# Kernel optimization log

Hardware: AMD Instinct MI355X
Metric: run time of the kernel (lower is better)

The kernel has to match this reference:

```python
import jax, jax.numpy as jnp
import numpy as np

NHEAD, HEAD_DIM = 10, 10
TEMPERATURE = 1.0
INV_SQRT_HD = np.float32(1.0 / np.sqrt(HEAD_DIM))


def setup_inputs() -> dict:
    key = jax.random.key(0)
    ks = jax.random.split(key, 6)
    B, nhid, L = 4, 128, 1024
    D = NHEAD * HEAD_DIM  # 100
    x = jax.random.normal(ks[0], (B, nhid, L, 1), dtype=jnp.float32)
    edge_matrix = jax.random.randint(ks[1], (B, L, L), 0, 2, dtype=jnp.int32)
    wq_w = jax.random.normal(ks[2], (D, nhid), dtype=jnp.float32) * 0.05
    wq_b = jnp.zeros((D,), jnp.float32)
    wedge_w = jax.random.normal(ks[3], (2 * HEAD_DIM,), dtype=jnp.float32) * 0.1
    wedge_b = jnp.zeros((1,), jnp.float32)
    wo_w = jax.random.normal(ks[4], (nhid, D), dtype=jnp.float32) * 0.05
    wo_b = jnp.zeros((nhid,), jnp.float32)
    return dict(x=x, edge_matrix=edge_matrix, wq_w=wq_w, wq_b=wq_b,
                wedge_w=wedge_w, wedge_b=wedge_b, wo_w=wo_w, wo_b=wo_b)


def reference(x, edge_matrix, wq_w, wq_b, wedge_w, wedge_b, wo_w, wo_b):
    B, nhid, L, _ = x.shape
    # WQ: 1x1 conv == per-position linear over channels
    q = jnp.einsum('bhl,ch->bcl', x[..., 0], wq_w) + wq_b[None, :, None]  # (B, nhead*hd, L)
    # source overwrites k and v with q (WK/WV dead code): k == v == q
    k = q.reshape(B, NHEAD, HEAD_DIM, L).transpose(0, 1, 3, 2)  # (B, nhead, L, hd)
    # WEDGE(Linear(2*hd,1)) over concat[k_i, k_j] == w1.k_i + w2.k_j + b (exact same math,
    # avoids materializing the O(L^2 * 2*hd) a_input tensor)
    s_i = jnp.einsum('bnld,d->bnl', k, wedge_w[:HEAD_DIM])
    s_j = jnp.einsum('bnld,d->bnl', k, wedge_w[HEAD_DIM:])
    alpha = (s_i[:, :, :, None] + s_j[:, :, None, :] + wedge_b[0]) * INV_SQRT_HD  # (B,nhead,L,L)
    alpha = jnp.where(edge_matrix[:, None, :, :] == 0, jnp.float32(-1e15), alpha)
    alpha = jax.nn.softmax(alpha, axis=-1) / TEMPERATURE  # dropout: identity at eval
    att = jnp.einsum('bnij,bnjd->bnid', alpha, k)  # v == k; (B, nhead, L, hd)
    # faithful to torch: raw row-major view(B, -1, L, 1) that scrambles (head,pos) ordering
    att = att.reshape(B, NHEAD * HEAD_DIM, L, 1)
    ret = jnp.einsum('bcl,oc->bol', att[..., 0], wo_w) + wo_b[None, :, None]
    ret = ret[..., None]  # (B, nhid, L, 1)
    return ret, alpha.reshape(B * NHEAD, L, L)
```

## Files before the change

### kernel.cpp

```cpp
#include <hip/hip_runtime.h>

#define BB   4
#define NHID 128
#define LL   1024
#define NH   10
#define HD   10
#define DD   100
#define SCALE 0.31622776601683794f

typedef float vfloat4 __attribute__((ext_vector_type(4)));

__global__ __launch_bounds__(256) void k_qproj(
    const float* __restrict__ x, const float* __restrict__ wq_w,
    const float* __restrict__ wq_b, float* __restrict__ kbuf) {
  const int l  = blockIdx.x * 256 + threadIdx.x;
  const int c0 = blockIdx.y * 2;
  const int b  = blockIdx.z;
  float acc0 = wq_b[c0], acc1 = wq_b[c0 + 1];
  const float* xb = x + (size_t)b * NHID * LL + l;
  const float* w0 = wq_w + (size_t)c0 * NHID;
  const float* w1 = w0 + NHID;
  #pragma unroll 8
  for (int h = 0; h < NHID; ++h) {
    float xv = xb[(size_t)h * LL];
    acc0 += w0[h] * xv;
    acc1 += w1[h] * xv;
  }
  {
    int c = c0, n = c / HD, d = c % HD;
    kbuf[(((size_t)(b * NH + n)) * LL + l) * HD + d] = acc0;
  }
  {
    int c = c0 + 1, n = c / HD, d = c % HD;
    kbuf[(((size_t)(b * NH + n)) * LL + l) * HD + d] = acc1;
  }
}

__global__ __launch_bounds__(256) void k_edgeproj(
    const float* __restrict__ kbuf, const float* __restrict__ we_w,
    float* __restrict__ esj) {
  const int idx = blockIdx.x * 256 + threadIdx.x;
  const float* kr = kbuf + (size_t)idx * HD;
  float s2 = 0.f;
  #pragma unroll
  for (int d = 0; d < HD; ++d) s2 += kr[d] * we_w[HD + d];
  esj[idx] = __expf(s2 * SCALE);
}

__global__ __launch_bounds__(256) void k_attn(
    const float* __restrict__ kbuf, const float* __restrict__ esj,
    const int* __restrict__ edge,
    float* __restrict__ alpha_out, float* __restrict__ att) {
  const int t    = threadIdx.x;
  const int lane = t & 63;
  const int wid  = t >> 6;
  const int blk  = blockIdx.x;
  const int rt   = blk & 63;
  const int bn   = blk >> 6;
  const int b    = bn / NH;
  const int i0   = rt * 16 + wid * 4;

  __shared__ float ks[LL * HD];
  {
    const float4* src = (const float4*)(kbuf + (size_t)bn * (LL * HD));
    float4* dst = (float4*)ks;
    for (int idx = t; idx < (LL * HD) / 4; idx += 256) dst[idx] = src[idx];
  }
  float  esv[16];
  float4 esv4[4];
  {
    const float* sp = esj + (size_t)bn * LL;
    #pragma unroll
    for (int m = 0; m < 16; ++m) esv[m] = sp[m * 64 + lane];
    const float4* sp4 = (const float4*)sp;
    #pragma unroll
    for (int m = 0; m < 4; ++m) esv4[m] = sp4[m * 64 + lane];
  }
  __syncthreads();

  const int* ebase = edge + (size_t)b * LL * LL;

  float part[4][HD];
  float denom[4];
  #pragma unroll
  for (int r = 0; r < 4; ++r) {
    denom[r] = 0.f;
    #pragma unroll
    for (int d = 0; d < HD; ++d) part[r][d] = 0.f;
  }
  #pragma unroll
  for (int m = 0; m < 16; ++m) {
    const float* kr = ks + (m * 64 + lane) * HD;
    float2 kv0 = *(const float2*)(kr + 0);
    float2 kv1 = *(const float2*)(kr + 2);
    float2 kv2 = *(const float2*)(kr + 4);
    float2 kv3 = *(const float2*)(kr + 6);
    float2 kv4 = *(const float2*)(kr + 8);
    const float es = esv[m];
    #pragma unroll
    for (int r = 0; r < 4; ++r) {
      int e = ebase[(size_t)(i0 + r) * LL + m * 64 + lane];
      float au = e ? es : 0.f;
      denom[r] += au;
      part[r][0] += au * kv0.x; part[r][1] += au * kv0.y;
      part[r][2] += au * kv1.x; part[r][3] += au * kv1.y;
      part[r][4] += au * kv2.x; part[r][5] += au * kv2.y;
      part[r][6] += au * kv3.x; part[r][7] += au * kv3.y;
      part[r][8] += au * kv4.x; part[r][9] += au * kv4.y;
    }
  }
  float inv[4];
  #pragma unroll
  for (int r = 0; r < 4; ++r) {
    float s = denom[r];
    #pragma unroll
    for (int sft = 32; sft >= 1; sft >>= 1) s += __shfl_xor(s, sft, 64);
    inv[r] = __builtin_amdgcn_rcpf(s);
  }

  float* ap = alpha_out + ((size_t)bn * LL + i0) * LL;
  #pragma unroll
  for (int m = 0; m < 4; ++m) {
    #pragma unroll
    for (int r = 0; r < 4; ++r) {
      int4 e = ((const int4*)(ebase + (size_t)(i0 + r) * LL))[m * 64 + lane];
      vfloat4 a;
      a.x = e.x ? esv4[m].x * inv[r] : 0.f;
      a.y = e.y ? esv4[m].y * inv[r] : 0.f;
      a.z = e.z ? esv4[m].z * inv[r] : 0.f;
      a.w = e.w ? esv4[m].w * inv[r] : 0.f;
      vfloat4* dst = (vfloat4*)(ap + (size_t)r * LL) + m * 64 + lane;
      __builtin_nontemporal_store(a, dst);
    }
  }

  const bool b5 = (lane & 32) != 0;
  const bool b4 = (lane & 16) != 0;
  const bool b3 = (lane & 8) != 0;
  const bool b2 = (lane & 4) != 0;
  #pragma unroll
  for (int r = 0; r < 4; ++r) {
    float pv[16];
    #pragma unroll
    for (int d = 0; d < HD; ++d) pv[d] = part[r][d];
    #pragma unroll
    for (int d = HD; d < 16; ++d) pv[d] = 0.f;
    #pragma unroll
    for (int i = 0; i < 8; ++i) {
      float snd = b5 ? pv[i] : pv[i + 8];
      float kp  = b5 ? pv[i + 8] : pv[i];
      pv[i] = kp + __shfl_xor(snd, 32, 64);
    }
    #pragma unroll
    for (int i = 0; i < 4; ++i) {
      float snd = b4 ? pv[i] : pv[i + 4];
      float kp  = b4 ? pv[i + 4] : pv[i];
      pv[i] = kp + __shfl_xor(snd, 16, 64);
    }
    #pragma unroll
    for (int i = 0; i < 2; ++i) {
      float snd = b3 ? pv[i] : pv[i + 2];
      float kp  = b3 ? pv[i + 2] : pv[i];
      pv[i] = kp + __shfl_xor(snd, 8, 64);
    }
    {
      float snd = b2 ? pv[0] : pv[1];
      float kp  = b2 ? pv[1] : pv[0];
      pv[0] = kp + __shfl_xor(snd, 4, 64);
    }
    pv[0] += __shfl_xor(pv[0], 2, 64);
    pv[0] += __shfl_xor(pv[0], 1, 64);
    float g = __shfl(pv[0], lane * 4, 64);
    if (lane < HD)
      att[((size_t)bn * LL + (i0 + r)) * HD + lane] = g * inv[r];
  }
}

__global__ __launch_bounds__(256) void k_out(
    const float* __restrict__ att, const float* __restrict__ wo_w,
    const float* __restrict__ wo_b, float* __restrict__ ret) {
  const int l  = blockIdx.x * 256 + threadIdx.x;
  const int o0 = blockIdx.y * 4;
  const int b  = blockIdx.z;
  const float* ab = att + (size_t)b * (DD * LL);
  float acc[4];
  #pragma unroll
  for (int oo = 0; oo < 4; ++oo) acc[oo] = wo_b[o0 + oo];
  for (int c = 0; c < DD; ++c) {
    float a = ab[(size_t)c * LL + l];
    #pragma unroll
    for (int oo = 0; oo < 4; ++oo) acc[oo] += wo_w[(size_t)(o0 + oo) * DD + c] * a;
  }
  #pragma unroll
  for (int oo = 0; oo < 4; ++oo)
    ret[((size_t)b * NHID + o0 + oo) * LL + l] = acc[oo];
}

extern "C" void kernel_launch(void* const* d_in, const int* in_sizes, int n_in,
                              void* d_out, int out_size, void* d_ws, size_t ws_size,
                              hipStream_t stream) {
  (void)in_sizes; (void)n_in; (void)out_size; (void)ws_size;
  const float* x    = (const float*)d_in[0];
  const int*   edge = (const int*)d_in[1];
  const float* wq_w = (const float*)d_in[2];
  const float* wq_b = (const float*)d_in[3];
  const float* we_w = (const float*)d_in[4];
  const float* wo_w = (const float*)d_in[6];
  const float* wo_b = (const float*)d_in[7];

  float* out       = (float*)d_out;
  float* ret_out   = out;
  float* alpha_out = out + (size_t)BB * NHID * LL;

  float* ws   = (float*)d_ws;
  float* kbuf = ws;
  float* esj  = kbuf + (size_t)BB * NH * LL * HD;
  float* att  = esj + (size_t)BB * NH * LL;

  dim3 g1(LL / 256, DD / 2, BB);
  k_qproj<<<g1, 256, 0, stream>>>(x, wq_w, wq_b, kbuf);

  k_edgeproj<<<(BB * NH * LL) / 256, 256, 0, stream>>>(kbuf, we_w, esj);

  k_attn<<<BB * NH * (LL / 16), 256, 0, stream>>>(kbuf, esj, edge, alpha_out, att);

  dim3 g3(LL / 256, NHID / 4, BB);
  k_out<<<g3, 256, 0, stream>>>(att, wo_w, wo_b, ret_out);
}
```

Baseline: 281.6 us.

## Transpose K layout, vectorize edge reads, cache edge mask, double rows per block

K is now stored transposed (head-dim major), so the attention kernel can read four consecutive key positions per lane as float4 from shared memory, and the edge matrix is read with int4 loads. The edge bits are packed into a per-row register mask during the first pass, so the alpha-writing pass no longer re-reads the edge matrix from global memory. Blocks grow to 512 threads covering 32 rows, which halves the number of times each head's K tile is staged into shared memory. The cost is higher register pressure from ten float4 key vectors per iteration and a different column interleaving in the reductions.

```diff
diff --git a/kernel.cpp b/kernel.cpp
--- a/kernel.cpp
+++ b/kernel.cpp
@@ -12,7 +12,7 @@
 
 __global__ __launch_bounds__(256) void k_qproj(
     const float* __restrict__ x, const float* __restrict__ wq_w,
-    const float* __restrict__ wq_b, float* __restrict__ kbuf) {
+    const float* __restrict__ wq_b, float* __restrict__ kT) {
   const int l  = blockIdx.x * 256 + threadIdx.x;
   const int c0 = blockIdx.y * 2;
   const int b  = blockIdx.z;
@@ -28,85 +28,84 @@
   }
   {
     int c = c0, n = c / HD, d = c % HD;
-    kbuf[(((size_t)(b * NH + n)) * LL + l) * HD + d] = acc0;
+    kT[(((size_t)(b * NH + n)) * HD + d) * LL + l] = acc0;
   }
   {
     int c = c0 + 1, n = c / HD, d = c % HD;
-    kbuf[(((size_t)(b * NH + n)) * LL + l) * HD + d] = acc1;
+    kT[(((size_t)(b * NH + n)) * HD + d) * LL + l] = acc1;
   }
 }
 
 __global__ __launch_bounds__(256) void k_edgeproj(
-    const float* __restrict__ kbuf, const float* __restrict__ we_w,
+    const float* __restrict__ kT, const float* __restrict__ we_w,
     float* __restrict__ esj) {
   const int idx = blockIdx.x * 256 + threadIdx.x;
-  const float* kr = kbuf + (size_t)idx * HD;
+  const int bn = idx >> 10, l = idx & (LL - 1);
+  const float* kp = kT + (size_t)bn * HD * LL + l;
   float s2 = 0.f;
   #pragma unroll
-  for (int d = 0; d < HD; ++d) s2 += kr[d] * we_w[HD + d];
+  for (int d = 0; d < HD; ++d) s2 += kp[(size_t)d * LL] * we_w[HD + d];
   esj[idx] = __expf(s2 * SCALE);
 }
 
-__global__ __launch_bounds__(256) void k_attn(
-    const float* __restrict__ kbuf, const float* __restrict__ esj,
+__global__ __launch_bounds__(512) void k_attn(
+    const float* __restrict__ kT, const float* __restrict__ esj,
     const int* __restrict__ edge,
     float* __restrict__ alpha_out, float* __restrict__ att) {
   const int t    = threadIdx.x;
   const int lane = t & 63;
   const int wid  = t >> 6;
   const int blk  = blockIdx.x;
-  const int rt   = blk & 63;
-  const int bn   = blk >> 6;
+  const int rt   = blk & 31;
+  const int bn   = blk >> 5;
   const int b    = bn / NH;
-  const int i0   = rt * 16 + wid * 4;
-
-  __shared__ float ks[LL * HD];
-  {
-    const float4* src = (const float4*)(kbuf + (size_t)bn * (LL * HD));
-    float4* dst = (float4*)ks;
-    for (int idx = t; idx < (LL * HD) / 4; idx += 256) dst[idx] = src[idx];
-  }
-  float  esv[16];
-  float4 esv4[4];
-  {
-    const float* sp = esj + (size_t)bn * LL;
-    #pragma unroll
-    for (int m = 0; m < 16; ++m) esv[m] = sp[m * 64 + lane];
-    const float4* sp4 = (const float4*)sp;
-    #pragma unroll
-    for (int m = 0; m < 4; ++m) esv4[m] = sp4[m * 64 + lane];
+  const int i0   = rt * 32 + wid * 4;
+
+  __shared__ float ksT[HD * LL];
+  {
+    const float4* src = (const float4*)(kT + (size_t)bn * (HD * LL));
+    float4* dst = (float4*)ksT;
+    #pragma unroll
+    for (int idx = t; idx < (HD * LL) / 4; idx += 512) dst[idx] = src[idx];
+  }
+  vfloat4 esv[4];
+  {
+    const vfloat4* sp = (const vfloat4*)(esj + (size_t)bn * LL);
+    #pragma unroll
+    for (int m = 0; m < 4; ++m) esv[m] = sp[m * 64 + lane];
   }
   __syncthreads();
 
-  const int* ebase = edge + (size_t)b * LL * LL;
+  const int* ebase = edge + (size_t)b * LL * LL + (size_t)i0 * LL;
 
   float part[4][HD];
   float denom[4];
+  unsigned mask[4];
   #pragma unroll
   for (int r = 0; r < 4; ++r) {
-    denom[r] = 0.f;
+    denom[r] = 0.f; mask[r] = 0u;
     #pragma unroll
     for (int d = 0; d < HD; ++d) part[r][d] = 0.f;
   }
   #pragma unroll
-  for (int m = 0; m < 16; ++m) {
-    const float* kr = ks + (m * 64 + lane) * HD;
-    float2 kv0 = *(const float2*)(kr + 0);
-    float2 kv1 = *(const float2*)(kr + 2);
-    float2 kv2 = *(const float2*)(kr + 4);
-    float2 kv3 = *(const float2*)(kr + 6);
-    float2 kv4 = *(const float2*)(kr + 8);
-    const float es = esv[m];
+  for (int m = 0; m < 4; ++m) {
+    vfloat4 kv[HD];
+    const float* kb = ksT + m * 256 + lane * 4;
+    #pragma unroll
+    for (int d = 0; d < HD; ++d) kv[d] = *(const vfloat4*)(kb + d * LL);
+    const vfloat4 es = esv[m];
     #pragma unroll
     for (int r = 0; r < 4; ++r) {
-      int e = ebase[(size_t)(i0 + r) * LL + m * 64 + lane];
-      float au = e ? es : 0.f;
-      denom[r] += au;
-      part[r][0] += au * kv0.x; part[r][1] += au * kv0.y;
-      part[r][2] += au * kv1.x; part[r][3] += au * kv1.y;
-      part[r][4] += au * kv2.x; part[r][5] += au * kv2.y;
-      part[r][6] += au * kv3.x; part[r][7] += au * kv3.y;
-      part[r][8] += au * kv4.x; part[r][9] += au * kv4.y;
+      int4 e = ((const int4*)(ebase + (size_t)r * LL))[m * 64 + lane];
+      float ax = e.x ? es.x : 0.f;
+      float ay = e.y ? es.y : 0.f;
+      float az = e.z ? es.z : 0.f;
+      float aw = e.w ? es.w : 0.f;
+      mask[r] |= ((e.x ? 1u : 0u) | (e.y ? 2u : 0u) | (e.z ? 4u : 0u) | (e.w ? 8u : 0u)) << (m * 4);
+      denom[r] += (ax + ay) + (az + aw);
+      #pragma unroll
+      for (int d = 0; d < HD; ++d)
+        part[r][d] += ax * kv[d].x + ay * kv[d].y + az * kv[d].z + aw * kv[d].w;
     }
   }
   float inv[4];
@@ -121,14 +120,15 @@
   float* ap = alpha_out + ((size_t)bn * LL + i0) * LL;
   #pragma unroll
   for (int m = 0; m < 4; ++m) {
+    const vfloat4 es = esv[m];
     #pragma unroll
     for (int r = 0; r < 4; ++r) {
-      int4 e = ((const int4*)(ebase + (size_t)(i0 + r) * LL))[m * 64 + lane];
+      const unsigned mk = mask[r] >> (m * 4);
       vfloat4 a;
-      a.x = e.x ? esv4[m].x * inv[r] : 0.f;
-      a.y = e.y ? esv4[m].y * inv[r] : 0.f;
-      a.z = e.z ? esv4[m].z * inv[r] : 0.f;
-      a.w = e.w ? esv4[m].w * inv[r] : 0.f;
+      a.x = (mk & 1u) ? es.x * inv[r] : 0.f;
+      a.y = (mk & 2u) ? es.y * inv[r] : 0.f;
+      a.z = (mk & 4u) ? es.z * inv[r] : 0.f;
+      a.w = (mk & 8u) ? es.w * inv[r] : 0.f;
       vfloat4* dst = (vfloat4*)(ap + (size_t)r * LL) + m * 64 + lane;
       __builtin_nontemporal_store(a, dst);
     }
@@ -213,16 +213,16 @@
   float* alpha_out = out + (size_t)BB * NHID * LL;
 
   float* ws   = (float*)d_ws;
-  float* kbuf = ws;
-  float* esj  = kbuf + (size_t)BB * NH * LL * HD;
+  float* kT   = ws;
+  float* esj  = kT + (size_t)BB * NH * HD * LL;
   float* att  = esj + (size_t)BB * NH * LL;
 
   dim3 g1(LL / 256, DD / 2, BB);
-  k_qproj<<<g1, 256, 0, stream>>>(x, wq_w, wq_b, kbuf);
-
-  k_edgeproj<<<(BB * NH * LL) / 256, 256, 0, stream>>>(kbuf, we_w, esj);
-
-  k_attn<<<BB * NH * (LL / 16), 256, 0, stream>>>(kbuf, esj, edge, alpha_out, att);
+  k_qproj<<<g1, 256, 0, stream>>>(x, wq_w, wq_b, kT);
+
+  k_edgeproj<<<(BB * NH * LL) / 256, 256, 0, stream>>>(kT, we_w, esj);
+
+  k_attn<<<BB * NH * (LL / 32), 512, 0, stream>>>(kT, esj, edge, alpha_out, att);
 
   dim3 g3(LL / 256, NHID / 4, BB);
   k_out<<<g3, 256, 0, stream>>>(att, wo_w, wo_b, ret_out);
```

New measurement: 255.3 us. -9.3%, faster.
